# Kernel tuning notes

Measured on AMD Instinct MI355X. Metric: run time of the kernel, lower is better.

## Reference

```python
import jax, jax.numpy as jnp
import numpy as np

TAO = 24
M = 7


def setup_inputs() -> dict:
    key = jax.random.key(0)
    k1, k2, k3 = jax.random.split(key, 3)
    B, S, C = 32, 2048, 7
    d_model = 512
    cm = C * (M + 1)  # 56 conv input channels
    x = jax.random.normal(k1, (B, S, C), dtype=jnp.float32)
    # total_conv: Conv1d(in=cm, out=d_model, kernel=3), kaiming_normal fan_in, leaky_relu
    fan_in = cm * 3
    gain = float(np.sqrt(2.0 / (1.0 + 0.01 ** 2)))
    std = gain / float(np.sqrt(fan_in))
    W = jax.random.normal(k2, (d_model, cm, 3), dtype=jnp.float32) * std
    bound = 1.0 / float(np.sqrt(fan_in))
    b = jax.random.uniform(k3, (d_model,), dtype=jnp.float32, minval=-bound, maxval=bound)
    return {"x": x, "W": W, "b": b}


def reference(x, W, b):
    B, S, C = x.shape
    mt = M * TAO  # delay-embedding lookback = 168
    n_valid = S - mt
    # sliding delay-embedding gather: for t in [mt, S), take x[t - k*tao] for k=0..M
    t_idx = jnp.arange(mt, S)                       # [n_valid]
    offs = jnp.arange(M + 1) * TAO                  # [M+1]
    tidx = t_idx[:, None] - offs[None, :]           # [n_valid, M+1]
    ext = x[:, tidx, :]                             # [B, n_valid, M+1, C]
    # torch reshape order: (n_valid, C, M+1) -> C major, offset minor
    fv = jnp.transpose(ext, (0, 1, 3, 2)).reshape(B, n_valid, C * (M + 1))
    # left-pad time axis with zeros to restore seq_len
    fv = jnp.pad(fv, ((0, 0), (mt, 0), (0, 0)))     # [B, S, C*(M+1)]
    # circular Conv1d (kernel 3, pad 1 circular)
    z = jnp.transpose(fv, (0, 2, 1))                # [B, C*(M+1), S]
    zp = jnp.pad(z, ((0, 0), (0, 0), (1, 1)), mode="wrap")
    out = jax.lax.conv_general_dilated(
        zp, W, window_strides=(1,), padding="VALID",
        dimension_numbers=("NCH", "OIH", "NCH"))    # [B, d_model, S]
    out = out + b[None, :, None]
    return jnp.transpose(out, (0, 2, 1))            # [B, S, d_model]
```

## Files before the change

kernel.cpp:

```cpp
#include <hip/hip_runtime.h>
#include <hip/hip_bf16.h>
#include <stdint.h>


#define TAO    24
#define MTAPS  7
#define C_IN   7
#define SEQ    2048
#define DMODEL 512
#define NROWS  65536
#define BO     128
#define BT     128
#define XROWS  298
#define XPLANE 304

typedef __attribute__((ext_vector_type(8))) short frag_ab;
typedef __attribute__((ext_vector_type(4))) float frag_cd;

__global__ __launch_bounds__(256)
void prep_w_kernel(const float* __restrict__ W, __hip_bfloat16* __restrict__ Wf)
{
    const int idx  = blockIdx.x * 256 + threadIdx.x;
    const int lane = idx & 63;
    const int kc   = (idx >> 6) & 1;
    const int oc   = (idx >> 7) & 31;
    const int h    = idx >> 12;
    const int o    = oc * 16 + (lane & 15);
    const int kof  = kc * 32 + (lane >> 4) * 8;

    union { __hip_bfloat16 s[8]; int4 v; } u;
#pragma unroll
    for (int j = 0; j < 8; j++) {
        const int k = kof + j;
        float v = (k < 56) ? W[o * 168 + k * 3 + h] : 0.0f;
        u.s[j] = __float2bfloat16(v);
    }
    ((int4*)Wf)[idx] = u.v;
}

__global__ __launch_bounds__(256, 3)
void gemm_kernel(const float* __restrict__ x,
                 const __hip_bfloat16* __restrict__ Wf,
                 const float* __restrict__ bias,
                 float* __restrict__ out)
{
    __shared__ short xt[8 * XPLANE];

    const int tid = threadIdx.x;
    const int bo  = blockIdx.x & 3;
    const int mb  = blockIdx.x >> 2;
    const int b   = mb >> 4;
    const int t0  = (mb & 15) * BT;
    const int o0  = bo * BO;

    {
        const float* xb = x + b * (SEQ * C_IN);
        const int base = (t0 - 169 + SEQ) & (SEQ - 1);
#pragma unroll
        for (int it = 0; it < 9; it++) {
            const int idx = it * 256 + tid;
            if (idx < XROWS * C_IN) {
                const int r = idx / 7;
                const int c = idx - r * 7;
                const int xrow = (base + r) & (SEQ - 1);
                const float v = xb[xrow * C_IN + c];
                __hip_bfloat16 bv = __float2bfloat16(v);
                xt[c * XPLANE + r] = *reinterpret_cast<short*>(&bv);
            }
        }
    }

    const int wave = tid >> 6;
    const int lane = tid & 63;
    const int wo   = (wave >> 1) * 64;
    const int wt   = (wave & 1) * 64;
    const int l15  = lane & 15;
    const int quad = lane >> 4;

    float4 bias4[4];
#pragma unroll
    for (int mi = 0; mi < 4; mi++)
        bias4[mi] = *(const float4*)&bias[o0 + wo + mi * 16 + quad * 4];

    frag_cd acc[4][4];
#pragma unroll
    for (int i = 0; i < 4; i++)
#pragma unroll
        for (int j = 0; j < 4; j++)
            acc[i][j] = (frag_cd){0.f, 0.f, 0.f, 0.f};

    __syncthreads();

    const int octile = bo * 8 + (wo >> 4);
#pragma unroll
    for (int h = 0; h < 3; h++) {
#pragma unroll
        for (int kc = 0; kc < 2; kc++) {
            const int qp = kc * 4 + quad;
            frag_ab wfr[4];
#pragma unroll
            for (int mi = 0; mi < 4; mi++) {
                const int tile = (h * 32 + octile + mi) * 2 + kc;
                wfr[mi] = *(const frag_ab*)((const char*)Wf + (size_t)tile * 1024 + lane * 16);
            }
            union { short s[8]; frag_ab f; int4 i4; } g[4];
#pragma unroll
            for (int ni = 0; ni < 4; ni++) {
                const int lbase = wt + ni * 16 + l15 + h;
                const int ttw = (t0 + lbase - 1 + SEQ) & (SEQ - 1);
                const short* p = &xt[qp * XPLANE + lbase];
#pragma unroll
                for (int j = 0; j < 8; j++)
                    g[ni].s[j] = p[168 - 24 * j];
                const bool valid = (ttw >= MTAPS * TAO) && (qp < 7);
                g[ni].i4.x = valid ? g[ni].i4.x : 0;
                g[ni].i4.y = valid ? g[ni].i4.y : 0;
                g[ni].i4.z = valid ? g[ni].i4.z : 0;
                g[ni].i4.w = valid ? g[ni].i4.w : 0;
            }
#pragma unroll
            for (int mi = 0; mi < 4; mi++)
#pragma unroll
                for (int ni = 0; ni < 4; ni++)
                    acc[mi][ni] = __builtin_amdgcn_mfma_f32_16x16x32_bf16(
                        wfr[mi], g[ni].f, acc[mi][ni], 0, 0, 0);
        }
    }

    const size_t rowbase = (size_t)b * SEQ + t0 + wt;
#pragma unroll
    for (int ni = 0; ni < 4; ni++) {
        const size_t r = rowbase + ni * 16 + l15;
        float* orow = out + r * DMODEL + o0 + wo + quad * 4;
#pragma unroll
        for (int mi = 0; mi < 4; mi++) {
            float4 v;
            v.x = acc[mi][ni][0] + bias4[mi].x;
            v.y = acc[mi][ni][1] + bias4[mi].y;
            v.z = acc[mi][ni][2] + bias4[mi].z;
            v.w = acc[mi][ni][3] + bias4[mi].w;
            *(float4*)(orow + mi * 16) = v;
        }
    }
}

#define KDIM  168
#define KPAD  192
#define FLDK  200
__global__ __launch_bounds__(256, 1)
void fused_tokenconv_kernel(const float* __restrict__ x,
                            const float* __restrict__ W,
                            const float* __restrict__ bias,
                            float* __restrict__ out)
{
    __shared__ __hip_bfloat16 As[128][FLDK];
    __shared__ __hip_bfloat16 Bs[128][FLDK];
    const int tid = threadIdx.x;
    const int blk = blockIdx.x;
    const int nb  = blk & 3;
    const int mb  = blk >> 2;
    const int b   = mb >> 4;
    const int t0  = (mb & 15) * 128;
    const int o0  = nb * 128;
    const float* xb = x + b * (SEQ * C_IN);

    for (int idx = tid; idx < 128 * KPAD; idx += 256) {
        int o_l = idx / KPAD;
        int i   = idx - o_l * KPAD;
        float v = (i < KDIM) ? W[(o0 + o_l) * KDIM + i] : 0.0f;
        Bs[o_l][i] = __float2bfloat16(v);
    }
    for (int idx = tid; idx < 128 * KPAD; idx += 256) {
        int t_l = idx / KPAD;
        int i   = idx - t_l * KPAD;
        float v = 0.0f;
        if (i < KDIM) {
            int c = i / 24;
            int r = i - c * 24;
            int m = r / 3;
            int h = r - m * 3;
            int s = (t0 + t_l + h - 1 + SEQ) & (SEQ - 1);
            if (s >= MTAPS * TAO) v = xb[(s - TAO * m) * C_IN + c];
        }
        As[t_l][i] = __float2bfloat16(v);
    }
    __syncthreads();

    const int wave = tid >> 6;
    const int lane = tid & 63;
    const int wm   = (wave >> 1) * 64;
    const int wn   = (wave & 1) * 64;
    const int l15  = lane & 15;
    const int quad = lane >> 4;

    frag_cd acc[4][4];
#pragma unroll
    for (int i = 0; i < 4; i++)
#pragma unroll
        for (int j = 0; j < 4; j++)
            acc[i][j] = (frag_cd){0.f, 0.f, 0.f, 0.f};

#pragma unroll
    for (int kc = 0; kc < KPAD / 32; kc++) {
        const int kof = kc * 32 + quad * 8;
        frag_ab a[4], bf[4];
#pragma unroll
        for (int mi = 0; mi < 4; mi++)
            a[mi] = *(const frag_ab*)&As[wm + mi * 16 + l15][kof];
#pragma unroll
        for (int ni = 0; ni < 4; ni++)
            bf[ni] = *(const frag_ab*)&Bs[wn + ni * 16 + l15][kof];
#pragma unroll
        for (int mi = 0; mi < 4; mi++)
#pragma unroll
            for (int ni = 0; ni < 4; ni++)
                acc[mi][ni] = __builtin_amdgcn_mfma_f32_16x16x32_bf16(
                    a[mi], bf[ni], acc[mi][ni], 0, 0, 0);
    }
    float* outb = out + (size_t)b * SEQ * DMODEL;
#pragma unroll
    for (int ni = 0; ni < 4; ni++) {
        const int o  = o0 + wn + ni * 16 + l15;
        const float bvv = bias[o];
#pragma unroll
        for (int mi = 0; mi < 4; mi++) {
#pragma unroll
            for (int reg = 0; reg < 4; reg++) {
                const int t = t0 + wm + mi * 16 + quad * 4 + reg;
                outb[(size_t)t * DMODEL + o] = acc[mi][ni][reg] + bvv;
            }
        }
    }
}

extern "C" void kernel_launch(void* const* d_in, const int* in_sizes, int n_in,
                              void* d_out, int out_size, void* d_ws, size_t ws_size,
                              hipStream_t stream) {
    const float* x    = (const float*)d_in[0];
    const float* W    = (const float*)d_in[1];
    const float* bias = (const float*)d_in[2];
    float* out        = (float*)d_out;

    const size_t w_bytes = (size_t)12288 * 16;
    if (ws_size >= w_bytes) {
        __hip_bfloat16* Wf = (__hip_bfloat16*)d_ws;
        hipLaunchKernelGGL(prep_w_kernel, dim3(48), dim3(256), 0, stream, W, Wf);
        hipLaunchKernelGGL(gemm_kernel, dim3((DMODEL / BO) * (NROWS / BT)), dim3(256), 0, stream,
                           x, Wf, bias, out);
    } else {
        hipLaunchKernelGGL(fused_tokenconv_kernel, dim3(32 * 16 * 4), dim3(256), 0, stream,
                           x, W, bias, out);
    }
}
```

Before: 154.2 us.

## Pre-gather delay-embedded MFMA B fragments into LDS for vector reads

The shared-memory staging now stores x as pre-gathered 8-element bf16 fragments per (channel, time) slot, with the validity mask applied once at fill time. The inner MFMA loop then does a single 16-byte LDS read per fragment instead of eight strided short reads plus per-fragment masking. The cost is a larger LDS footprint (about 17 KB against about 5 KB) and more global loads during the fill, since each x element is read several times, which may lower occupancy. The bias load is also moved after the main loop to shorten register live ranges.

```diff
diff --git a/kernel.cpp b/kernel.cpp
--- a/kernel.cpp
+++ b/kernel.cpp
@@ -11,8 +11,8 @@
 #define NROWS  65536
 #define BO     128
 #define BT     128
-#define XROWS  298
-#define XPLANE 304
+#define GROWS  130
+#define GPLANE 1056
 
 typedef __attribute__((ext_vector_type(8))) short frag_ab;
 typedef __attribute__((ext_vector_type(4))) float frag_cd;
@@ -44,7 +44,7 @@
                  const float* __restrict__ bias,
                  float* __restrict__ out)
 {
-    __shared__ short xt[8 * XPLANE];
+    __shared__ __align__(16) short gt[8 * GPLANE];
 
     const int tid = threadIdx.x;
     const int bo  = blockIdx.x & 3;
@@ -55,17 +55,25 @@
 
     {
         const float* xb = x + b * (SEQ * C_IN);
-        const int base = (t0 - 169 + SEQ) & (SEQ - 1);
-#pragma unroll
-        for (int it = 0; it < 9; it++) {
+#pragma unroll
+        for (int it = 0; it < 5; it++) {
             const int idx = it * 256 + tid;
-            if (idx < XROWS * C_IN) {
-                const int r = idx / 7;
-                const int c = idx - r * 7;
-                const int xrow = (base + r) & (SEQ - 1);
-                const float v = xb[xrow * C_IN + c];
-                __hip_bfloat16 bv = __float2bfloat16(v);
-                xt[c * XPLANE + r] = *reinterpret_cast<short*>(&bv);
+            if (idx < 8 * GROWS) {
+                const int qp = idx / GROWS;
+                const int lb = idx - qp * GROWS;
+                const int ttw = (t0 + lb - 1 + SEQ) & (SEQ - 1);
+                union { short s[8]; int4 v; } u;
+                if ((ttw >= MTAPS * TAO) && (qp < 7)) {
+                    const float* p = xb + ttw * C_IN + qp;
+#pragma unroll
+                    for (int j = 0; j < 8; j++) {
+                        __hip_bfloat16 bv = __float2bfloat16(p[-168 * j]);
+                        u.s[j] = *reinterpret_cast<short*>(&bv);
+                    }
+                } else {
+                    u.v = (int4){0, 0, 0, 0};
+                }
+                *(int4*)&gt[qp * GPLANE + lb * 8] = u.v;
             }
         }
     }
@@ -77,11 +85,6 @@
     const int l15  = lane & 15;
     const int quad = lane >> 4;
 
-    float4 bias4[4];
-#pragma unroll
-    for (int mi = 0; mi < 4; mi++)
-        bias4[mi] = *(const float4*)&bias[o0 + wo + mi * 16 + quad * 4];
-
     frag_cd acc[4][4];
 #pragma unroll
     for (int i = 0; i < 4; i++)
@@ -103,29 +106,24 @@
                 const int tile = (h * 32 + octile + mi) * 2 + kc;
                 wfr[mi] = *(const frag_ab*)((const char*)Wf + (size_t)tile * 1024 + lane * 16);
             }
-            union { short s[8]; frag_ab f; int4 i4; } g[4];
-#pragma unroll
-            for (int ni = 0; ni < 4; ni++) {
-                const int lbase = wt + ni * 16 + l15 + h;
-                const int ttw = (t0 + lbase - 1 + SEQ) & (SEQ - 1);
-                const short* p = &xt[qp * XPLANE + lbase];
-#pragma unroll
-                for (int j = 0; j < 8; j++)
-                    g[ni].s[j] = p[168 - 24 * j];
-                const bool valid = (ttw >= MTAPS * TAO) && (qp < 7);
-                g[ni].i4.x = valid ? g[ni].i4.x : 0;
-                g[ni].i4.y = valid ? g[ni].i4.y : 0;
-                g[ni].i4.z = valid ? g[ni].i4.z : 0;
-                g[ni].i4.w = valid ? g[ni].i4.w : 0;
-            }
+            const short* gp = &gt[qp * GPLANE + (wt + l15 + h) * 8];
+            frag_ab g[4];
+#pragma unroll
+            for (int ni = 0; ni < 4; ni++)
+                g[ni] = *(const frag_ab*)(gp + ni * 128);
 #pragma unroll
             for (int mi = 0; mi < 4; mi++)
 #pragma unroll
                 for (int ni = 0; ni < 4; ni++)
                     acc[mi][ni] = __builtin_amdgcn_mfma_f32_16x16x32_bf16(
-                        wfr[mi], g[ni].f, acc[mi][ni], 0, 0, 0);
-        }
-    }
+                        wfr[mi], g[ni], acc[mi][ni], 0, 0, 0);
+        }
+    }
+
+    float4 bias4[4];
+#pragma unroll
+    for (int mi = 0; mi < 4; mi++)
+        bias4[mi] = *(const float4*)&bias[o0 + wo + mi * 16 + quad * 4];
 
     const size_t rowbase = (size_t)b * SEQ + t0 + wt;
 #pragma unroll
```

After: 155.3 us. No clear change (+0.8%).

## Reorder K dimension to time-major so B fragments load as vectors from LDS

Applied to the files above, without the earlier changes.

Changes the shared-memory x tile from channel-planar to row-major with 8 bf16 per time row, and permutes the packed weight K ordering to (tap-major, channel-minor) so that each B fragment is a single 16-byte LDS read instead of eight scalar gathers. The x staging becomes one vector store per row, boundary masking is limited to edge tiles, bias loading moves after the main loop, and launch bounds are raised to 4 blocks per CU. The intent is to cut LDS instruction count and register pressure. The risk is LDS bank conflicts from the 16-byte row stride and correctness depending on the matching weight permutation.

```diff
diff --git a/kernel.cpp b/kernel.cpp
--- a/kernel.cpp
+++ b/kernel.cpp
@@ -12,7 +12,7 @@
 #define BO     128
 #define BT     128
 #define XROWS  298
-#define XPLANE 304
+#define XLD    8
 
 typedef __attribute__((ext_vector_type(8))) short frag_ab;
 typedef __attribute__((ext_vector_type(4))) float frag_cd;
@@ -31,20 +31,22 @@
     union { __hip_bfloat16 s[8]; int4 v; } u;
 #pragma unroll
     for (int j = 0; j < 8; j++) {
-        const int k = kof + j;
-        float v = (k < 56) ? W[o * 168 + k * 3 + h] : 0.0f;
+        const int kp = kof + j;
+        const int m  = kp >> 3;
+        const int c  = kp & 7;
+        float v = (c < 7) ? W[o * 168 + (c * 8 + m) * 3 + h] : 0.0f;
         u.s[j] = __float2bfloat16(v);
     }
     ((int4*)Wf)[idx] = u.v;
 }
 
-__global__ __launch_bounds__(256, 3)
+__global__ __launch_bounds__(256, 4)
 void gemm_kernel(const float* __restrict__ x,
                  const __hip_bfloat16* __restrict__ Wf,
                  const float* __restrict__ bias,
                  float* __restrict__ out)
 {
-    __shared__ short xt[8 * XPLANE];
+    __shared__ __align__(16) short xt[304 * XLD];
 
     const int tid = threadIdx.x;
     const int bo  = blockIdx.x & 3;
@@ -57,15 +59,19 @@
         const float* xb = x + b * (SEQ * C_IN);
         const int base = (t0 - 169 + SEQ) & (SEQ - 1);
 #pragma unroll
-        for (int it = 0; it < 9; it++) {
-            const int idx = it * 256 + tid;
-            if (idx < XROWS * C_IN) {
-                const int r = idx / 7;
-                const int c = idx - r * 7;
+        for (int it = 0; it < 2; it++) {
+            const int r = it * 256 + tid;
+            if (r < XROWS) {
                 const int xrow = (base + r) & (SEQ - 1);
-                const float v = xb[xrow * C_IN + c];
-                __hip_bfloat16 bv = __float2bfloat16(v);
-                xt[c * XPLANE + r] = *reinterpret_cast<short*>(&bv);
+                const float* p = xb + xrow * C_IN;
+                union { short s[8]; int4 v; } u;
+#pragma unroll
+                for (int c = 0; c < 7; c++) {
+                    __hip_bfloat16 bv = __float2bfloat16(p[c]);
+                    u.s[c] = *reinterpret_cast<short*>(&bv);
+                }
+                u.s[7] = 0;
+                *(int4*)&xt[r * XLD] = u.v;
             }
         }
     }
@@ -77,11 +83,6 @@
     const int l15  = lane & 15;
     const int quad = lane >> 4;
 
-    float4 bias4[4];
-#pragma unroll
-    for (int mi = 0; mi < 4; mi++)
-        bias4[mi] = *(const float4*)&bias[o0 + wo + mi * 16 + quad * 4];
-
     frag_cd acc[4][4];
 #pragma unroll
     for (int i = 0; i < 4; i++)
@@ -91,32 +92,36 @@
 
     __syncthreads();
 
+    const bool edge = (t0 <= MTAPS * TAO) || (t0 == (SEQ - BT));
     const int octile = bo * 8 + (wo >> 4);
+
 #pragma unroll
     for (int h = 0; h < 3; h++) {
 #pragma unroll
         for (int kc = 0; kc < 2; kc++) {
-            const int qp = kc * 4 + quad;
+            const int m = kc * 4 + quad;
             frag_ab wfr[4];
 #pragma unroll
             for (int mi = 0; mi < 4; mi++) {
                 const int tile = (h * 32 + octile + mi) * 2 + kc;
                 wfr[mi] = *(const frag_ab*)((const char*)Wf + (size_t)tile * 1024 + lane * 16);
             }
-            union { short s[8]; frag_ab f; int4 i4; } g[4];
-#pragma unroll
-            for (int ni = 0; ni < 4; ni++) {
-                const int lbase = wt + ni * 16 + l15 + h;
-                const int ttw = (t0 + lbase - 1 + SEQ) & (SEQ - 1);
-                const short* p = &xt[qp * XPLANE + lbase];
-#pragma unroll
-                for (int j = 0; j < 8; j++)
-                    g[ni].s[j] = p[168 - 24 * j];
-                const bool valid = (ttw >= MTAPS * TAO) && (qp < 7);
-                g[ni].i4.x = valid ? g[ni].i4.x : 0;
-                g[ni].i4.y = valid ? g[ni].i4.y : 0;
-                g[ni].i4.z = valid ? g[ni].i4.z : 0;
-                g[ni].i4.w = valid ? g[ni].i4.w : 0;
+            const short* gp = &xt[(wt + l15 + h + 168 - 24 * m) * XLD];
+            union { frag_ab f; int4 i4; } g[4];
+#pragma unroll
+            for (int ni = 0; ni < 4; ni++)
+                g[ni].f = *(const frag_ab*)(gp + ni * 16 * XLD);
+            if (edge) {
+#pragma unroll
+                for (int ni = 0; ni < 4; ni++) {
+                    const int lb  = wt + ni * 16 + l15 + h;
+                    const int ttw = (t0 + lb - 1 + SEQ) & (SEQ - 1);
+                    const bool valid = (ttw >= MTAPS * TAO);
+                    g[ni].i4.x = valid ? g[ni].i4.x : 0;
+                    g[ni].i4.y = valid ? g[ni].i4.y : 0;
+                    g[ni].i4.z = valid ? g[ni].i4.z : 0;
+                    g[ni].i4.w = valid ? g[ni].i4.w : 0;
+                }
             }
 #pragma unroll
             for (int mi = 0; mi < 4; mi++)
@@ -126,6 +131,11 @@
                         wfr[mi], g[ni].f, acc[mi][ni], 0, 0, 0);
         }
     }
+
+    float4 bias4[4];
+#pragma unroll
+    for (int mi = 0; mi < 4; mi++)
+        bias4[mi] = *(const float4*)&bias[o0 + wo + mi * 16 + quad * 4];
 
     const size_t rowbase = (size_t)b * SEQ + t0 + wt;
 #pragma unroll
```

Result: slower. 164.4 us (+6.7%).
